# Performance work log

Hardware: AMD Instinct MI355X
Metric: run time of the kernel (lower is better)

## Reference

```python
import math
import jax, jax.numpy as jnp
import numpy as np

T, N, D = 8, 1024, 128  # num_timestamps, tot_nodes, node_input_size

def setup_inputs() -> dict:
    key = jax.random.key(0)
    k1, k2 = jax.random.split(key)
    raw_features = jax.random.normal(k1, (T, N, D), dtype=jnp.float32)
    adj = jax.random.randint(k2, (N, N), 0, 2, dtype=jnp.int32)
    return {"raw_features": raw_features, "adj": adj}

def reference(raw_features, adj):
    t, n, d = raw_features.shape
    scale = 1.0 / math.sqrt(d)
    # --- GAT: adjacency-masked self-attention per timestamp ---
    scores = jnp.einsum('tnd,tmd->tnm', raw_features, raw_features) * scale  # [T,N,N]
    masked = jnp.where(adj[None] > 0, scores, jnp.float32(-1e12))
    attention = jax.nn.softmax(masked, axis=2)
    node_features = jnp.einsum('tnm,tmd->tnd', attention, raw_features)      # [T,N,D]
    # --- temporal scores per node ---
    spatial_features = node_features.transpose(1, 0, 2)                      # [N,T,D]
    temp_scores = jnp.einsum('ntd,nsd->nts', spatial_features, spatial_features) * scale
    spatial_weights = jax.nn.sigmoid(temp_scores)                            # [N,T,T]
    # --- repeat(N,1,1).view(N,N,T,T) == broadcast over leading axis: ST[i,j] = sw[j] ---
    ST = jnp.broadcast_to(spatial_weights[None], (n, n, t, t))               # [N,N,T,T]
    ST = ST.transpose(3, 1, 2, 0)                                            # [T,N,T,N]
    return ST.reshape(t * n, t * n)
```

## Files before the change

kernel.cpp:

```cpp
#include <hip/hip_runtime.h>
#include <hip/hip_bf16.h>
#include <math.h>

#define T 8
#define N 1024
#define D 128

constexpr float SCALE = 0.08838834764831845f;

typedef __attribute__((ext_vector_type(8))) short short8;
typedef __attribute__((ext_vector_type(4))) float floatx4;

__global__ __launch_bounds__(256) void convert_bf16(const float* __restrict__ X,
                                                    ushort* __restrict__ XB) {
    int idx = blockIdx.x * 256 + threadIdx.x;
    float4 v = ((const float4*)X)[idx];
    ushort4 o;
    __hip_bfloat16 h;
    h = __float2bfloat16(v.x); o.x = *(ushort*)&h;
    h = __float2bfloat16(v.y); o.y = *(ushort*)&h;
    h = __float2bfloat16(v.z); o.z = *(ushort*)&h;
    h = __float2bfloat16(v.w); o.w = *(ushort*)&h;
    ((ushort4*)XB)[idx] = o;
}

__global__ __launch_bounds__(256) void gemm1_mfma(const ushort* __restrict__ XB,
                                                  const int* __restrict__ adj,
                                                  float* __restrict__ S) {
    const int wid  = threadIdx.x >> 6;
    const int lane = threadIdx.x & 63;
    const int gw   = blockIdx.x * 4 + wid;
    const int t    = gw >> 8;
    const int tile = gw & 255;
    const int i0 = (tile >> 4) * 64;
    const int j0 = (tile & 15) * 64;
    const int m = lane & 15, quad = lane >> 4;

    const ushort* Xt = XB + (size_t)t * N * D;

    const ushort* pa[4];
    const ushort* pb[4];
    #pragma unroll
    for (int r = 0; r < 4; ++r) {
        pa[r] = Xt + (size_t)(i0 + 16 * r + m) * D + quad * 8;
        pb[r] = Xt + (size_t)(j0 + 16 * r + m) * D + quad * 8;
    }

    floatx4 acc[4][4] = {};
    #pragma unroll
    for (int kq = 0; kq < 4; ++kq) {
        short8 a[4], b[4];
        #pragma unroll
        for (int r = 0; r < 4; ++r) {
            a[r] = *(const short8*)(pa[r] + kq * 32);
            b[r] = *(const short8*)(pb[r] + kq * 32);
        }
        #pragma unroll
        for (int r = 0; r < 4; ++r)
            #pragma unroll
            for (int c = 0; c < 4; ++c)
                acc[r][c] = __builtin_amdgcn_mfma_f32_16x16x32_bf16(a[r], b[c], acc[r][c], 0, 0, 0);
    }

    float* St = S + (size_t)t * N * N;
    #pragma unroll
    for (int r = 0; r < 4; ++r) {
        #pragma unroll
        for (int q = 0; q < 4; ++q) {
            const int i = i0 + 16 * r + quad * 4 + q;
            const int* arow = adj + (size_t)i * N;
            float* srow = St + (size_t)i * N;
            #pragma unroll
            for (int c = 0; c < 4; ++c) {
                const int j = j0 + 16 * c + m;
                float v = acc[r][c][q] * SCALE;
                srow[j] = (arow[j] != 0) ? v : -1e12f;
            }
        }
    }
}

__global__ __launch_bounds__(256) void softmax_rows(float* __restrict__ S) {
    const int row  = blockIdx.x * 4 + (threadIdx.x >> 6);
    const int lane = threadIdx.x & 63;
    float4* pv = (float4*)(S + (size_t)row * N);

    float4 v[4];
    float mx = -INFINITY;
    #pragma unroll
    for (int q = 0; q < 4; ++q) {
        v[q] = pv[q * 64 + lane];
        mx = fmaxf(mx, fmaxf(fmaxf(v[q].x, v[q].y), fmaxf(v[q].z, v[q].w)));
    }
    #pragma unroll
    for (int off = 32; off > 0; off >>= 1) mx = fmaxf(mx, __shfl_xor(mx, off));

    float sum = 0.f;
    #pragma unroll
    for (int q = 0; q < 4; ++q) {
        v[q].x = __expf(v[q].x - mx); v[q].y = __expf(v[q].y - mx);
        v[q].z = __expf(v[q].z - mx); v[q].w = __expf(v[q].w - mx);
        sum += v[q].x + v[q].y + v[q].z + v[q].w;
    }
    #pragma unroll
    for (int off = 32; off > 0; off >>= 1) sum += __shfl_xor(sum, off);
    const float inv = 1.f / sum;

    #pragma unroll
    for (int q = 0; q < 4; ++q) {
        v[q].x *= inv; v[q].y *= inv; v[q].z *= inv; v[q].w *= inv;
        pv[q * 64 + lane] = v[q];
    }
}

__global__ __launch_bounds__(256) void gemm2(const float* __restrict__ P,
                                             const float* __restrict__ X,
                                             float* __restrict__ NF) {
    const int t  = blockIdx.y;
    const int i0 = blockIdx.x * 16;
    const float* At = P + (size_t)t * N * N;
    const float* Xt = X + (size_t)t * N * D;

    __shared__ float Ps[16 * 36];
    __shared__ float Xs[32 * 132];

    const int tid = threadIdx.x;
    const int tx = tid & 31, ty = tid >> 5;

    float4 acc0 = {0.f, 0.f, 0.f, 0.f};
    float4 acc1 = {0.f, 0.f, 0.f, 0.f};

    for (int kc = 0; kc < N; kc += 32) {
        if (tid < 128) {
            int r = tid >> 3, c4 = (tid & 7) * 4;
            *(float4*)(Ps + r * 36 + c4) = *(const float4*)(At + (size_t)(i0 + r) * N + kc + c4);
        }
        #pragma unroll
        for (int p = 0; p < 4; ++p) {
            int idx = tid + p * 256;
            int r = idx >> 5, c4 = (idx & 31) * 4;
            *(float4*)(Xs + r * 132 + c4) = *(const float4*)(Xt + (size_t)(kc + r) * D + c4);
        }
        __syncthreads();
        #pragma unroll
        for (int k4 = 0; k4 < 8; ++k4) {
            float4 a0 = *(const float4*)(Ps + (ty * 2 + 0) * 36 + k4 * 4);
            float4 a1 = *(const float4*)(Ps + (ty * 2 + 1) * 36 + k4 * 4);
            const float a0v[4] = {a0.x, a0.y, a0.z, a0.w};
            const float a1v[4] = {a1.x, a1.y, a1.z, a1.w};
            #pragma unroll
            for (int j = 0; j < 4; ++j) {
                float4 x4 = *(const float4*)(Xs + (k4 * 4 + j) * 132 + tx * 4);
                acc0.x += a0v[j] * x4.x; acc0.y += a0v[j] * x4.y;
                acc0.z += a0v[j] * x4.z; acc0.w += a0v[j] * x4.w;
                acc1.x += a1v[j] * x4.x; acc1.y += a1v[j] * x4.y;
                acc1.z += a1v[j] * x4.z; acc1.w += a1v[j] * x4.w;
            }
        }
        __syncthreads();
    }

    float* NFt = NF + (size_t)t * N * D;
    *(float4*)(NFt + (size_t)(i0 + ty * 2 + 0) * D + tx * 4) = acc0;
    *(float4*)(NFt + (size_t)(i0 + ty * 2 + 1) * D + tx * 4) = acc1;
}

__global__ __launch_bounds__(64) void temporal(const float* __restrict__ NF,
                                               float* __restrict__ SW) {
    const int j = blockIdx.x;
    __shared__ float F[T][D];
    const int tid = threadIdx.x;
    #pragma unroll
    for (int p = 0; p < 4; ++p) {
        int idx = tid + p * 64;
        int a = idx >> 5, c4 = (idx & 31) * 4;
        *(float4*)(&F[a][c4]) = *(const float4*)(NF + ((size_t)a * N + j) * D + c4);
    }
    __syncthreads();
    const int a = tid >> 3, b = tid & 7;
    float s = 0.f;
    #pragma unroll
    for (int d4 = 0; d4 < 32; ++d4) {
        float4 fa = *(const float4*)(&F[a][d4 * 4]);
        float4 fb = *(const float4*)(&F[b][d4 * 4]);
        s += fa.x * fb.x + fa.y * fb.y + fa.z * fb.z + fa.w * fb.w;
    }
    s *= SCALE;
    SW[(size_t)j * 64 + tid] = 1.f / (1.f + __expf(-s));
}

__global__ __launch_bounds__(256) void expand(const float* __restrict__ SW,
                                              float* __restrict__ out) {
    const int row = blockIdx.x;
    const int b = row >> 10, j = row & 1023;
    const int tid = threadIdx.x;
    float4* orow = (float4*)(out + (size_t)row * (T * N));
    #pragma unroll
    for (int a = 0; a < T; ++a) {
        float w = SW[(size_t)j * 64 + a * 8 + b];
        orow[a * 256 + tid] = make_float4(w, w, w, w);
    }
}

extern "C" void kernel_launch(void* const* d_in, const int* in_sizes, int n_in,
                              void* d_out, int out_size, void* d_ws, size_t ws_size,
                              hipStream_t stream) {
    const float* X   = (const float*)d_in[0];
    const int*   adj = (const int*)d_in[1];
    float* out = (float*)d_out;

    float* S   = (float*)d_ws;
    float* NF  = S + (size_t)T * N * N;
    float* SW  = NF + (size_t)T * N * D;
    ushort* XB = (ushort*)(SW + (size_t)N * T * T);

    convert_bf16<<<dim3(T * N * D / 4 / 256), 256, 0, stream>>>(X, XB);
    gemm1_mfma<<<dim3(512), 256, 0, stream>>>(XB, adj, S);
    softmax_rows<<<dim3(T * N / 4), 256, 0, stream>>>(S);
    gemm2<<<dim3(N / 16, T), 256, 0, stream>>>(S, X, NF);
    temporal<<<dim3(N), 64, 0, stream>>>(NF, SW);
    expand<<<dim3(T * N), 256, 0, stream>>>(SW, out);
}
```

Measured before the change: 370.4 us.

## Fuse score GEMM, masked softmax and PV GEMM into one MFMA kernel

```diff
diff --git a/kernel.cpp b/kernel.cpp
--- a/kernel.cpp
+++ b/kernel.cpp
@@ -11,158 +11,182 @@
 typedef __attribute__((ext_vector_type(8))) short short8;
 typedef __attribute__((ext_vector_type(4))) float floatx4;
 
+#define MFMA16(a, b, c) __builtin_amdgcn_mfma_f32_16x16x32_bf16((a), (b), (c), 0, 0, 0)
+
 __global__ __launch_bounds__(256) void convert_bf16(const float* __restrict__ X,
-                                                    ushort* __restrict__ XB) {
+                                                    ushort* __restrict__ XB,
+                                                    ushort* __restrict__ XBT_hi,
+                                                    ushort* __restrict__ XBT_lo) {
     int idx = blockIdx.x * 256 + threadIdx.x;
     float4 v = ((const float4*)X)[idx];
+    int row = idx >> 5;
+    int d0  = (idx & 31) * 4;
+    int t = row >> 10, n = row & 1023;
+    float vv[4] = {v.x, v.y, v.z, v.w};
     ushort4 o;
-    __hip_bfloat16 h;
-    h = __float2bfloat16(v.x); o.x = *(ushort*)&h;
-    h = __float2bfloat16(v.y); o.y = *(ushort*)&h;
-    h = __float2bfloat16(v.z); o.z = *(ushort*)&h;
-    h = __float2bfloat16(v.w); o.w = *(ushort*)&h;
+    ushort* op = (ushort*)&o;
+    #pragma unroll
+    for (int k = 0; k < 4; ++k) {
+        __hip_bfloat16 h = __float2bfloat16(vv[k]);
+        float hf = __bfloat162float(h);
+        __hip_bfloat16 l = __float2bfloat16(vv[k] - hf);
+        op[k] = *(ushort*)&h;
+        size_t toff = ((size_t)t * D + d0 + k) * N + n;
+        XBT_hi[toff] = *(ushort*)&h;
+        XBT_lo[toff] = *(ushort*)&l;
+    }
     ((ushort4*)XB)[idx] = o;
 }
 
-__global__ __launch_bounds__(256) void gemm1_mfma(const ushort* __restrict__ XB,
+__global__ __launch_bounds__(256) void attn_fused(const ushort* __restrict__ XB,
+                                                  const ushort* __restrict__ XBT_hi,
+                                                  const ushort* __restrict__ XBT_lo,
                                                   const int* __restrict__ adj,
-                                                  float* __restrict__ S) {
-    const int wid  = threadIdx.x >> 6;
-    const int lane = threadIdx.x & 63;
-    const int gw   = blockIdx.x * 4 + wid;
-    const int t    = gw >> 8;
-    const int tile = gw & 255;
-    const int i0 = (tile >> 4) * 64;
-    const int j0 = (tile & 15) * 64;
-    const int m = lane & 15, quad = lane >> 4;
-
-    const ushort* Xt = XB + (size_t)t * N * D;
-
-    const ushort* pa[4];
-    const ushort* pb[4];
-    #pragma unroll
-    for (int r = 0; r < 4; ++r) {
-        pa[r] = Xt + (size_t)(i0 + 16 * r + m) * D + quad * 8;
-        pb[r] = Xt + (size_t)(j0 + 16 * r + m) * D + quad * 8;
-    }
-
-    floatx4 acc[4][4] = {};
-    #pragma unroll
-    for (int kq = 0; kq < 4; ++kq) {
-        short8 a[4], b[4];
-        #pragma unroll
-        for (int r = 0; r < 4; ++r) {
-            a[r] = *(const short8*)(pa[r] + kq * 32);
-            b[r] = *(const short8*)(pb[r] + kq * 32);
-        }
-        #pragma unroll
-        for (int r = 0; r < 4; ++r)
-            #pragma unroll
-            for (int c = 0; c < 4; ++c)
-                acc[r][c] = __builtin_amdgcn_mfma_f32_16x16x32_bf16(a[r], b[c], acc[r][c], 0, 0, 0);
-    }
-
-    float* St = S + (size_t)t * N * N;
-    #pragma unroll
-    for (int r = 0; r < 4; ++r) {
-        #pragma unroll
-        for (int q = 0; q < 4; ++q) {
-            const int i = i0 + 16 * r + quad * 4 + q;
-            const int* arow = adj + (size_t)i * N;
-            float* srow = St + (size_t)i * N;
-            #pragma unroll
-            for (int c = 0; c < 4; ++c) {
-                const int j = j0 + 16 * c + m;
-                float v = acc[r][c][q] * SCALE;
-                srow[j] = (arow[j] != 0) ? v : -1e12f;
-            }
-        }
-    }
-}
-
-__global__ __launch_bounds__(256) void softmax_rows(float* __restrict__ S) {
-    const int row  = blockIdx.x * 4 + (threadIdx.x >> 6);
-    const int lane = threadIdx.x & 63;
-    float4* pv = (float4*)(S + (size_t)row * N);
-
-    float4 v[4];
-    float mx = -INFINITY;
-    #pragma unroll
-    for (int q = 0; q < 4; ++q) {
-        v[q] = pv[q * 64 + lane];
-        mx = fmaxf(mx, fmaxf(fmaxf(v[q].x, v[q].y), fmaxf(v[q].z, v[q].w)));
-    }
-    #pragma unroll
-    for (int off = 32; off > 0; off >>= 1) mx = fmaxf(mx, __shfl_xor(mx, off));
-
-    float sum = 0.f;
-    #pragma unroll
-    for (int q = 0; q < 4; ++q) {
-        v[q].x = __expf(v[q].x - mx); v[q].y = __expf(v[q].y - mx);
-        v[q].z = __expf(v[q].z - mx); v[q].w = __expf(v[q].w - mx);
-        sum += v[q].x + v[q].y + v[q].z + v[q].w;
-    }
-    #pragma unroll
-    for (int off = 32; off > 0; off >>= 1) sum += __shfl_xor(sum, off);
-    const float inv = 1.f / sum;
-
-    #pragma unroll
-    for (int q = 0; q < 4; ++q) {
-        v[q].x *= inv; v[q].y *= inv; v[q].z *= inv; v[q].w *= inv;
-        pv[q * 64 + lane] = v[q];
-    }
-}
-
-__global__ __launch_bounds__(256) void gemm2(const float* __restrict__ P,
-                                             const float* __restrict__ X,
-                                             float* __restrict__ NF) {
+                                                  float* __restrict__ NF) {
     const int t  = blockIdx.y;
     const int i0 = blockIdx.x * 16;
-    const float* At = P + (size_t)t * N * N;
-    const float* Xt = X + (size_t)t * N * D;
-
-    __shared__ float Ps[16 * 36];
-    __shared__ float Xs[32 * 132];
-
-    const int tid = threadIdx.x;
-    const int tx = tid & 31, ty = tid >> 5;
-
-    float4 acc0 = {0.f, 0.f, 0.f, 0.f};
-    float4 acc1 = {0.f, 0.f, 0.f, 0.f};
-
-    for (int kc = 0; kc < N; kc += 32) {
-        if (tid < 128) {
-            int r = tid >> 3, c4 = (tid & 7) * 4;
-            *(float4*)(Ps + r * 36 + c4) = *(const float4*)(At + (size_t)(i0 + r) * N + kc + c4);
-        }
-        #pragma unroll
-        for (int p = 0; p < 4; ++p) {
-            int idx = tid + p * 256;
-            int r = idx >> 5, c4 = (idx & 31) * 4;
-            *(float4*)(Xs + r * 132 + c4) = *(const float4*)(Xt + (size_t)(kc + r) * D + c4);
-        }
-        __syncthreads();
-        #pragma unroll
-        for (int k4 = 0; k4 < 8; ++k4) {
-            float4 a0 = *(const float4*)(Ps + (ty * 2 + 0) * 36 + k4 * 4);
-            float4 a1 = *(const float4*)(Ps + (ty * 2 + 1) * 36 + k4 * 4);
-            const float a0v[4] = {a0.x, a0.y, a0.z, a0.w};
-            const float a1v[4] = {a1.x, a1.y, a1.z, a1.w};
-            #pragma unroll
-            for (int j = 0; j < 4; ++j) {
-                float4 x4 = *(const float4*)(Xs + (k4 * 4 + j) * 132 + tx * 4);
-                acc0.x += a0v[j] * x4.x; acc0.y += a0v[j] * x4.y;
-                acc0.z += a0v[j] * x4.z; acc0.w += a0v[j] * x4.w;
-                acc1.x += a1v[j] * x4.x; acc1.y += a1v[j] * x4.y;
-                acc1.z += a1v[j] * x4.z; acc1.w += a1v[j] * x4.w;
-            }
-        }
-        __syncthreads();
+    const int tid  = threadIdx.x;
+    const int wid  = tid >> 6;
+    const int lane = tid & 63;
+    const int m    = lane & 15;
+    const int quad = lane >> 4;
+    const int jbase = wid * 256;
+
+    __shared__ ushort Ph[16][1024];
+    __shared__ ushort Plo[16][1024];
+    float* red = (float*)&Ph[0][0];
+
+    const ushort* Xt = XB + (size_t)t * N * D;
+
+    short8 afrag[4];
+    {
+        const ushort* pa = Xt + (size_t)(i0 + m) * D + quad * 8;
+        #pragma unroll
+        for (int kq = 0; kq < 4; ++kq) afrag[kq] = *(const short8*)(pa + kq * 32);
+    }
+
+    floatx4 acc[16];
+    #pragma unroll
+    for (int c = 0; c < 16; ++c) acc[c] = (floatx4){0.f, 0.f, 0.f, 0.f};
+
+    #pragma unroll
+    for (int c = 0; c < 16; ++c) {
+        const ushort* pb = Xt + (size_t)(jbase + 16 * c + m) * D + quad * 8;
+        short8 b0 = *(const short8*)(pb);
+        short8 b1 = *(const short8*)(pb + 32);
+        short8 b2 = *(const short8*)(pb + 64);
+        short8 b3 = *(const short8*)(pb + 96);
+        acc[c] = MFMA16(afrag[0], b0, acc[c]);
+        acc[c] = MFMA16(afrag[1], b1, acc[c]);
+        acc[c] = MFMA16(afrag[2], b2, acc[c]);
+        acc[c] = MFMA16(afrag[3], b3, acc[c]);
+    }
+
+    #pragma unroll
+    for (int q = 0; q < 4; ++q) {
+        const int i = i0 + quad * 4 + q;
+        const int* arow = adj + (size_t)i * N + jbase + m;
+        #pragma unroll
+        for (int c = 0; c < 16; ++c) {
+            int a = arow[16 * c];
+            acc[c][q] = (a != 0) ? acc[c][q] * SCALE : -1e12f;
+        }
+    }
+
+    float mx[4], inv[4];
+    #pragma unroll
+    for (int q = 0; q < 4; ++q) {
+        float v_ = acc[0][q];
+        #pragma unroll
+        for (int c = 1; c < 16; ++c) v_ = fmaxf(v_, acc[c][q]);
+        v_ = fmaxf(v_, __shfl_xor(v_, 1));
+        v_ = fmaxf(v_, __shfl_xor(v_, 2));
+        v_ = fmaxf(v_, __shfl_xor(v_, 4));
+        v_ = fmaxf(v_, __shfl_xor(v_, 8));
+        mx[q] = v_;
+    }
+    if (m == 0) {
+        #pragma unroll
+        for (int q = 0; q < 4; ++q) red[wid * 16 + quad * 4 + q] = mx[q];
+    }
+    __syncthreads();
+    #pragma unroll
+    for (int q = 0; q < 4; ++q) {
+        int r = quad * 4 + q;
+        mx[q] = fmaxf(fmaxf(red[r], red[16 + r]), fmaxf(red[32 + r], red[48 + r]));
+    }
+
+    float sm[4];
+    #pragma unroll
+    for (int q = 0; q < 4; ++q) {
+        float s_ = 0.f;
+        #pragma unroll
+        for (int c = 0; c < 16; ++c) {
+            float p = __expf(acc[c][q] - mx[q]);
+            acc[c][q] = p;
+            s_ += p;
+        }
+        s_ += __shfl_xor(s_, 1);
+        s_ += __shfl_xor(s_, 2);
+        s_ += __shfl_xor(s_, 4);
+        s_ += __shfl_xor(s_, 8);
+        sm[q] = s_;
+    }
+    if (m == 0) {
+        #pragma unroll
+        for (int q = 0; q < 4; ++q) red[64 + wid * 16 + quad * 4 + q] = sm[q];
+    }
+    __syncthreads();
+    #pragma unroll
+    for (int q = 0; q < 4; ++q) {
+        int r = quad * 4 + q;
+        inv[q] = 1.f / (red[64 + r] + red[80 + r] + red[96 + r] + red[112 + r]);
+    }
+    __syncthreads();
+
+    #pragma unroll
+    for (int q = 0; q < 4; ++q) {
+        const int row = quad * 4 + q;
+        #pragma unroll
+        for (int c = 0; c < 16; ++c) {
+            const int col = jbase + 16 * c + m;
+            const int sc = ((((col >> 3) ^ (row & 7)) << 3) | (col & 7));
+            float p = acc[c][q] * inv[q];
+            __hip_bfloat16 h = __float2bfloat16(p);
+            float hf = __bfloat162float(h);
+            __hip_bfloat16 l = __float2bfloat16(p - hf);
+            Ph[row][sc]  = *(ushort*)&h;
+            Plo[row][sc] = *(ushort*)&l;
+        }
+    }
+    __syncthreads();
+
+    floatx4 accN[2];
+    accN[0] = (floatx4){0.f, 0.f, 0.f, 0.f};
+    accN[1] = (floatx4){0.f, 0.f, 0.f, 0.f};
+    const int f0 = wid * 32;
+    #pragma unroll 4
+    for (int kq = 0; kq < 32; ++kq) {
+        const int blk = (((kq * 4 + quad) ^ (m & 7)) << 3);
+        short8 ah = *(const short8*)&Ph[m][blk];
+        short8 al = *(const short8*)&Plo[m][blk];
+        #pragma unroll
+        for (int nt = 0; nt < 2; ++nt) {
+            size_t off = ((size_t)t * D + f0 + nt * 16 + m) * N + kq * 32 + quad * 8;
+            short8 bh = *(const short8*)(XBT_hi + off);
+            short8 bl = *(const short8*)(XBT_lo + off);
+            accN[nt] = MFMA16(ah, bh, accN[nt]);
+            accN[nt] = MFMA16(ah, bl, accN[nt]);
+            accN[nt] = MFMA16(al, bh, accN[nt]);
+        }
     }
 
     float* NFt = NF + (size_t)t * N * D;
-    *(float4*)(NFt + (size_t)(i0 + ty * 2 + 0) * D + tx * 4) = acc0;
-    *(float4*)(NFt + (size_t)(i0 + ty * 2 + 1) * D + tx * 4) = acc1;
+    #pragma unroll
+    for (int nt = 0; nt < 2; ++nt)
+        #pragma unroll
+        for (int q = 0; q < 4; ++q)
+            NFt[(size_t)(i0 + quad * 4 + q) * D + f0 + nt * 16 + m] = accN[nt][q];
 }
 
 __global__ __launch_bounds__(64) void temporal(const float* __restrict__ NF,
@@ -209,15 +233,14 @@
     const int*   adj = (const int*)d_in[1];
     float* out = (float*)d_out;
 
-    float* S   = (float*)d_ws;
-    float* NF  = S + (size_t)T * N * N;
-    float* SW  = NF + (size_t)T * N * D;
-    ushort* XB = (ushort*)(SW + (size_t)N * T * T);
-
-    convert_bf16<<<dim3(T * N * D / 4 / 256), 256, 0, stream>>>(X, XB);
-    gemm1_mfma<<<dim3(512), 256, 0, stream>>>(XB, adj, S);
-    softmax_rows<<<dim3(T * N / 4), 256, 0, stream>>>(S);
-    gemm2<<<dim3(N / 16, T), 256, 0, stream>>>(S, X, NF);
+    float*  NF     = (float*)d_ws;
+    float*  SW     = NF + (size_t)T * N * D;
+    ushort* XB     = (ushort*)(SW + (size_t)N * T * T);
+    ushort* XBT_hi = XB + (size_t)T * N * D;
+    ushort* XBT_lo = XBT_hi + (size_t)T * N * D;
+
+    convert_bf16<<<dim3(T * N * D / 4 / 256), 256, 0, stream>>>(X, XB, XBT_hi, XBT_lo);
+    attn_fused<<<dim3(N / 16, T), 256, 0, stream>>>(XB, XBT_hi, XBT_lo, adj, NF);
     temporal<<<dim3(N), 64, 0, stream>>>(NF, SW);
     expand<<<dim3(T * N), 256, 0, stream>>>(SW, out);
 }
```

Result: faster. 341.0 us (-7.9%).
